# Kernel tuning notes

Hardware: AMD Instinct MI355X
Metric: run time of the kernel (lower is better)

The kernel has to match this reference:

```python
import jax, jax.numpy as jnp
import numpy as np

KS = 21        # kernel_size
SIGMA = 5.0    # sigma
C = 3          # channels
PAD = KS // 2  # reflection pad = 10


def _gaussian_kernel():
    # Matches torch construction: 2D isotropic Gaussian on integer grid, then
    # normalized to sum 1. Separable => outer product of 1D Gaussians.
    coords = jnp.arange(KS, dtype=jnp.float32)
    mean = (KS - 1) / 2.0
    g1 = jnp.exp(-((coords - mean) ** 2) / (2.0 * SIGMA ** 2))
    k2 = jnp.outer(g1, g1)
    k2 = k2 / jnp.sum(k2)
    # depthwise weight [C, 1, KS, KS] (OIHW with feature_group_count=C)
    return jnp.tile(k2[None, None, :, :], (C, 1, 1, 1))


def setup_inputs() -> dict:
    key = jax.random.key(0)
    x = jax.random.normal(key, (32, 3, 512, 512), dtype=jnp.float32)
    return {"x": x}


def reference(x):
    w = _gaussian_kernel()
    xp = jnp.pad(x, ((0, 0), (0, 0), (PAD, PAD), (PAD, PAD)), mode="reflect")
    out = jax.lax.conv_general_dilated(
        xp, w,
        window_strides=(1, 1),
        padding="VALID",
        dimension_numbers=("NCHW", "OIHW", "NCHW"),
        feature_group_count=C,
    )
    return out  # [B, C, H, W], same spatial size as input
```

## Files before the change

### kernel.cpp

```cpp
#include <hip/hip_runtime.h>
#include <math.h>


#define KS   21
#define PAD  10
#define TILE 64
#define LW   (TILE + 2 * PAD)
#define IMG_H 512
#define IMG_W 512
#define NTHREADS 256

__global__ __launch_bounds__(NTHREADS) void gauss_blur_kernel(
    const float* __restrict__ in, float* __restrict__ out)
{
    __shared__ float s_in[LW * LW];
    __shared__ float s_h[LW * TILE];

    float w[KS];
    {
        float s = 0.f;
#pragma unroll
        for (int k = 0; k < KS; ++k) {
            float d = (float)(k - PAD);
            w[k] = expf(-d * d * (1.0f / 50.0f));
            s += w[k];
        }
        float inv = 1.0f / s;
#pragma unroll
        for (int k = 0; k < KS; ++k) w[k] *= inv;
    }

    const int tid   = threadIdx.x;
    const int plane = blockIdx.z;
    const int x0    = blockIdx.x * TILE;
    const int y0    = blockIdx.y * TILE;

    const float* __restrict__ pin = in + (size_t)plane * (IMG_H * IMG_W);

    for (int idx = tid; idx < LW * LW; idx += NTHREADS) {
        int ly = idx / LW;
        int lx = idx - ly * LW;
        int gy = y0 + ly - PAD;
        int gx = x0 + lx - PAD;
        gy = (gy < 0) ? -gy : ((gy >= IMG_H) ? (2 * IMG_H - 2 - gy) : gy);
        gx = (gx < 0) ? -gx : ((gx >= IMG_W) ? (2 * IMG_W - 2 - gx) : gx);
        s_in[idx] = pin[gy * IMG_W + gx];
    }
    __syncthreads();

    for (int idx = tid; idx < LW * TILE; idx += NTHREADS) {
        int ly = idx >> 6;
        int lx = idx & 63;
        const float* row = &s_in[ly * LW + lx];
        float acc = 0.f;
#pragma unroll
        for (int k = 0; k < KS; ++k) acc += w[k] * row[k];
        s_h[idx] = acc;
    }
    __syncthreads();

    float* __restrict__ pout = out + (size_t)plane * (IMG_H * IMG_W);
    for (int idx = tid; idx < TILE * TILE; idx += NTHREADS) {
        int oy = idx >> 6;
        int ox = idx & 63;
        const float* col = &s_h[oy * TILE + ox];
        float acc = 0.f;
#pragma unroll
        for (int k = 0; k < KS; ++k) acc += w[k] * col[k * TILE];
        pout[(size_t)(y0 + oy) * IMG_W + (x0 + ox)] = acc;
    }
}

extern "C" void kernel_launch(void* const* d_in, const int* in_sizes, int n_in,
                              void* d_out, int out_size, void* d_ws, size_t ws_size,
                              hipStream_t stream)
{
    const float* x = (const float*)d_in[0];
    float* out = (float*)d_out;

    dim3 grid(IMG_W / TILE, IMG_H / TILE, 96);
    dim3 block(NTHREADS);
    gauss_blur_kernel<<<grid, block, 0, stream>>>(x, out);
}
```

Measured before the change: 237.7 us.

## Register-block both blur passes with float4 LDS loads and 4x4 output tiles

The horizontal pass now makes each thread compute four adjacent outputs from one 24-float register window loaded with float4 LDS reads. The vertical pass gives each thread a 4x4 output block, reusing each loaded row across four output rows and storing with float4 global writes. This cuts LDS traffic and load instruction count per FMA. The cost is higher register pressure, and the float4 LDS access patterns may cause bank conflicts.

```diff
diff --git a/kernel.cpp b/kernel.cpp
--- a/kernel.cpp
+++ b/kernel.cpp
@@ -13,8 +13,8 @@
 __global__ __launch_bounds__(NTHREADS) void gauss_blur_kernel(
     const float* __restrict__ in, float* __restrict__ out)
 {
-    __shared__ float s_in[LW * LW];
-    __shared__ float s_h[LW * TILE];
+    __shared__ __align__(16) float s_in[LW * LW];
+    __shared__ __align__(16) float s_h[LW * TILE];
 
     float w[KS];
     {
@@ -48,26 +48,56 @@
     }
     __syncthreads();
 
-    for (int idx = tid; idx < LW * TILE; idx += NTHREADS) {
-        int ly = idx >> 6;
-        int lx = idx & 63;
-        const float* row = &s_in[ly * LW + lx];
-        float acc = 0.f;
+    for (int idx = tid; idx < LW * (TILE / 4); idx += NTHREADS) {
+        int ly = idx >> 4;
+        int lx = (idx & 15) << 2;
+        const float4* rp = (const float4*)&s_in[ly * LW + lx];
+        float v[24];
 #pragma unroll
-        for (int k = 0; k < KS; ++k) acc += w[k] * row[k];
-        s_h[idx] = acc;
+        for (int t = 0; t < 6; ++t) {
+            float4 f = rp[t];
+            v[4 * t + 0] = f.x; v[4 * t + 1] = f.y;
+            v[4 * t + 2] = f.z; v[4 * t + 3] = f.w;
+        }
+        float a0 = 0.f, a1 = 0.f, a2 = 0.f, a3 = 0.f;
+#pragma unroll
+        for (int k = 0; k < KS; ++k) {
+            float wk = w[k];
+            a0 += wk * v[k + 0];
+            a1 += wk * v[k + 1];
+            a2 += wk * v[k + 2];
+            a3 += wk * v[k + 3];
+        }
+        *(float4*)&s_h[ly * TILE + lx] = make_float4(a0, a1, a2, a3);
     }
     __syncthreads();
 
-    float* __restrict__ pout = out + (size_t)plane * (IMG_H * IMG_W);
-    for (int idx = tid; idx < TILE * TILE; idx += NTHREADS) {
-        int oy = idx >> 6;
-        int ox = idx & 63;
-        const float* col = &s_h[oy * TILE + ox];
-        float acc = 0.f;
+    {
+        const int rg = tid >> 4;
+        const int cg = tid & 15;
+        const int oy = rg << 2;
+        const int ox = cg << 2;
+
+        float4 r0 = make_float4(0, 0, 0, 0);
+        float4 r1 = make_float4(0, 0, 0, 0);
+        float4 r2 = make_float4(0, 0, 0, 0);
+        float4 r3 = make_float4(0, 0, 0, 0);
+
 #pragma unroll
-        for (int k = 0; k < KS; ++k) acc += w[k] * col[k * TILE];
-        pout[(size_t)(y0 + oy) * IMG_W + (x0 + ox)] = acc;
+        for (int t = 0; t < KS + 3; ++t) {
+            float4 c = *(const float4*)&s_h[(oy + t) * TILE + ox];
+            if (t - 0 >= 0 && t - 0 < KS) { float wk = w[t - 0]; r0.x += wk * c.x; r0.y += wk * c.y; r0.z += wk * c.z; r0.w += wk * c.w; }
+            if (t - 1 >= 0 && t - 1 < KS) { float wk = w[t - 1]; r1.x += wk * c.x; r1.y += wk * c.y; r1.z += wk * c.z; r1.w += wk * c.w; }
+            if (t - 2 >= 0 && t - 2 < KS) { float wk = w[t - 2]; r2.x += wk * c.x; r2.y += wk * c.y; r2.z += wk * c.z; r2.w += wk * c.w; }
+            if (t - 3 >= 0 && t - 3 < KS) { float wk = w[t - 3]; r3.x += wk * c.x; r3.y += wk * c.y; r3.z += wk * c.z; r3.w += wk * c.w; }
+        }
+
+        float* __restrict__ pout = out + (size_t)plane * (IMG_H * IMG_W)
+                                       + (size_t)(y0 + oy) * IMG_W + (x0 + ox);
+        *(float4*)&pout[0 * IMG_W] = r0;
+        *(float4*)&pout[1 * IMG_W] = r1;
+        *(float4*)&pout[2 * IMG_W] = r2;
+        *(float4*)&pout[3 * IMG_W] = r3;
     }
 }
 
```

After: 229.5 us. 3.4% less time.

## Register-block separable blur passes and vectorize interior tile loads

Applied to the files above, without the earlier changes.

Interior tiles now load the input halo with float4 global reads into a 16-byte-aligned, padded shared buffer. Only the image-edge tiles keep the scalar reflect path. The horizontal pass gives each thread 8 outputs computed from 32 register-cached values. The vertical pass gives each thread a 16-row column strip that slides over 36 shared-memory rows, so each loaded value feeds several outputs. Together these cut shared-memory traffic and index arithmetic per output, at the cost of higher register pressure and a more complex load path.

```diff
diff --git a/kernel.cpp b/kernel.cpp
--- a/kernel.cpp
+++ b/kernel.cpp
@@ -5,7 +5,9 @@
 #define KS   21
 #define PAD  10
 #define TILE 64
-#define LW   (TILE + 2 * PAD)
+#define LH   (TILE + 2 * PAD)
+#define SW_IN 88
+#define SW_H  68
 #define IMG_H 512
 #define IMG_W 512
 #define NTHREADS 256
@@ -13,8 +15,8 @@
 __global__ __launch_bounds__(NTHREADS) void gauss_blur_kernel(
     const float* __restrict__ in, float* __restrict__ out)
 {
-    __shared__ float s_in[LW * LW];
-    __shared__ float s_h[LW * TILE];
+    __shared__ __align__(16) float s_in[LH * SW_IN];
+    __shared__ __align__(16) float s_h [LH * SW_H];
 
     float w[KS];
     {
@@ -37,37 +39,77 @@
 
     const float* __restrict__ pin = in + (size_t)plane * (IMG_H * IMG_W);
 
-    for (int idx = tid; idx < LW * LW; idx += NTHREADS) {
-        int ly = idx / LW;
-        int lx = idx - ly * LW;
-        int gy = y0 + ly - PAD;
-        int gx = x0 + lx - PAD;
-        gy = (gy < 0) ? -gy : ((gy >= IMG_H) ? (2 * IMG_H - 2 - gy) : gy);
-        gx = (gx < 0) ? -gx : ((gx >= IMG_W) ? (2 * IMG_W - 2 - gx) : gx);
-        s_in[idx] = pin[gy * IMG_W + gx];
+    const bool x_interior = (blockIdx.x != 0) && (blockIdx.x != (IMG_W / TILE - 1));
+    if (x_interior) {
+        for (int q = tid; q < LH * (SW_IN / 4); q += NTHREADS) {
+            int ly  = q / (SW_IN / 4);
+            int lx4 = q - ly * (SW_IN / 4);
+            int col = lx4 << 2;
+            int gy  = y0 + ly - PAD;
+            gy = (gy < 0) ? -gy : ((gy >= IMG_H) ? (2 * IMG_H - 2 - gy) : gy);
+            float4 f = *(const float4*)&pin[(size_t)gy * IMG_W + (x0 - 12) + col];
+            *(float4*)&s_in[ly * SW_IN + col] = f;
+        }
+    } else {
+        for (int q = tid; q < LH * SW_IN; q += NTHREADS) {
+            int ly = q / SW_IN;
+            int lx = q - ly * SW_IN;
+            int gy = y0 + ly - PAD;
+            int gx = x0 + lx - 12;
+            gy = (gy < 0) ? -gy : ((gy >= IMG_H) ? (2 * IMG_H - 2 - gy) : gy);
+            gx = (gx < 0) ? -gx : ((gx >= IMG_W) ? (2 * IMG_W - 2 - gx) : gx);
+            s_in[ly * SW_IN + lx] = pin[(size_t)gy * IMG_W + gx];
+        }
     }
     __syncthreads();
 
-    for (int idx = tid; idx < LW * TILE; idx += NTHREADS) {
-        int ly = idx >> 6;
-        int lx = idx & 63;
-        const float* row = &s_in[ly * LW + lx];
-        float acc = 0.f;
+    for (int it = 0; it < 3; ++it) {
+        int idx = tid + it * NTHREADS;
+        if (idx < LH * (TILE / 8)) {
+            int ly = idx >> 3;
+            int lx = (idx & 7) << 3;
+            const float4* rp = (const float4*)&s_in[ly * SW_IN + lx];
+            float v[32];
 #pragma unroll
-        for (int k = 0; k < KS; ++k) acc += w[k] * row[k];
-        s_h[idx] = acc;
+            for (int t = 0; t < 8; ++t) {
+                float4 f = rp[t];
+                v[4 * t + 0] = f.x; v[4 * t + 1] = f.y;
+                v[4 * t + 2] = f.z; v[4 * t + 3] = f.w;
+            }
+            float a[8] = {0, 0, 0, 0, 0, 0, 0, 0};
+#pragma unroll
+            for (int k = 0; k < KS; ++k) {
+                float wk = w[k];
+#pragma unroll
+                for (int j = 0; j < 8; ++j) a[j] += wk * v[2 + j + k];
+            }
+            *(float4*)&s_h[ly * SW_H + lx]     = make_float4(a[0], a[1], a[2], a[3]);
+            *(float4*)&s_h[ly * SW_H + lx + 4] = make_float4(a[4], a[5], a[6], a[7]);
+        }
     }
     __syncthreads();
 
-    float* __restrict__ pout = out + (size_t)plane * (IMG_H * IMG_W);
-    for (int idx = tid; idx < TILE * TILE; idx += NTHREADS) {
-        int oy = idx >> 6;
-        int ox = idx & 63;
-        const float* col = &s_h[oy * TILE + ox];
-        float acc = 0.f;
+    {
+        const int wv = tid >> 6;
+        const int x  = tid & 63;
+        const int oy = wv << 4;
+
+        float acc[16];
 #pragma unroll
-        for (int k = 0; k < KS; ++k) acc += w[k] * col[k * TILE];
-        pout[(size_t)(y0 + oy) * IMG_W + (x0 + ox)] = acc;
+        for (int j = 0; j < 16; ++j) acc[j] = 0.f;
+
+#pragma unroll
+        for (int t = 0; t < 36; ++t) {
+            float r = s_h[(oy + t) * SW_H + x];
+#pragma unroll
+            for (int j = 0; j < 16; ++j)
+                if (j >= t - (KS - 1) && j <= t) acc[j] += w[t - j] * r;
+        }
+
+        float* __restrict__ pout = out + (size_t)plane * (IMG_H * IMG_W)
+                                       + (size_t)(y0 + oy) * IMG_W + x0 + x;
+#pragma unroll
+        for (int j = 0; j < 16; ++j) pout[(size_t)j * IMG_W] = acc[j];
     }
 }
 
```

Measured after the change: 230.3 us. -3.1%, faster.
